# Kernel tuning notes

Measured on AMD Instinct MI355X. Metric: run time of the kernel, lower is better.

The kernel has to match this reference:

```python
import jax, jax.numpy as jnp
import numpy as np
from jax import lax

PS = 4  # patchsize

def conv2d(x, w, b, pad, dil=1):
    y = lax.conv_general_dilated(x, w, (1, 1), [(pad, pad), (pad, pad)],
                                 rhs_dilation=(dil, dil),
                                 dimension_numbers=('NCHW', 'OIHW', 'NCHW'))
    return y + b[None, :, None, None]

def instance_norm(x, eps=1e-5):
    mu = x.mean(axis=(2, 3), keepdims=True)
    var = x.var(axis=(2, 3), keepdims=True)
    return (x - mu) / jnp.sqrt(var + eps)

def lrelu(x):
    return jnp.where(x >= 0, x, 0.2 * x)

def setup_inputs() -> dict:
    key = jax.random.key(0)
    ks = jax.random.split(key, 20)
    B, C, H, W = 16, 256, 64, 64
    nh, nw = H // PS, W // PS
    N = nh * nw
    s = 0.05
    return {
        'x': jax.random.normal(ks[0], (B, C, H, W), jnp.float32),
        'mask': jax.random.uniform(ks[1], (B, 1, H, W), jnp.float32),
        'dis': jax.random.normal(ks[2], (N, N), jnp.float32),
        'lap_a': jnp.ones((1,), jnp.float32),
        'Wq': jax.random.normal(ks[3], (C, C, 1, 1), jnp.float32) * s,
        'bq': jax.random.normal(ks[4], (C,), jnp.float32) * s,
        'Wk': jax.random.normal(ks[5], (C, C, 1, 1), jnp.float32) * s,
        'bk': jax.random.normal(ks[6], (C,), jnp.float32) * s,
        'Wv': jax.random.normal(ks[7], (C, C, 1, 1), jnp.float32) * s,
        'bv': jax.random.normal(ks[8], (C,), jnp.float32) * s,
        'noise_q': jax.random.normal(ks[9], (B, C, nh, PS, nw, PS), jnp.float32),
        'noise_k': jax.random.normal(ks[10], (B, C, nh, PS, nw, PS), jnp.float32),
        'noise_v': jax.random.normal(ks[11], (B, C, nh, PS, nw, PS), jnp.float32),
        'W_out': jax.random.normal(ks[12], (C, C, 3, 3), jnp.float32) * s,
        'b_out': jax.random.normal(ks[13], (C,), jnp.float32) * s,
        'W1': jax.random.normal(ks[14], (C, C, 3, 3), jnp.float32) * s,
        'b1': jax.random.normal(ks[15], (C,), jnp.float32) * s,
        'W2': jax.random.normal(ks[16], (C, C, 3, 3), jnp.float32) * s,
        'b2': jax.random.normal(ks[17], (C,), jnp.float32) * s,
    }

def _patchify(t, noise, B, C, nh, nw):
    # (B,C,H,W) -> (B,C,nh,PS,nw,PS) + noise -> (B, nh*nw, C*PS*PS)
    t = t.reshape(B, C, nh, PS, nw, PS) + noise
    t = t.transpose(0, 2, 4, 1, 3, 5).reshape(B, nh * nw, C * PS * PS)
    return t

def reference(x, mask, dis, lap_a, Wq, bq, Wk, bk, Wv, bv,
              noise_q, noise_k, noise_v, W_out, b_out, W1, b1, W2, b2):
    B, C, H, W = x.shape
    nh, nw = H // PS, W // PS
    N = nh * nw
    head = PS * 4
    Cp = C * PS * PS
    d = Cp // head

    residual = x
    q = _patchify(conv2d(x, Wq, bq, 0), noise_q, B, C, nh, nw)
    k = _patchify(conv2d(x, Wk, bk, 0), noise_k, B, C, nh, nw)
    v = _patchify(conv2d(x, Wv, bv, 0), noise_v, B, C, nh, nw)

    dis_b = jax.nn.softplus(lap_a)[0] * dis  # (N, N)

    qh = q.reshape(B, N, head, d)
    kh = k.reshape(B, N, head, d)
    vh = v.reshape(B, N, head, d)

    # scores: (head, B, N, N); bias added BEFORE scaling, as in the original
    scores = jnp.einsum('bnhd,bmhd->hbnm', qh, kh)
    scores = (scores + dis_b) / jnp.sqrt(jnp.asarray(d, scores.dtype))

    # mask: patch mean < 0.5 masks key positions
    m = mask.reshape(B, 1, nh, PS, nw, PS).transpose(0, 2, 4, 1, 3, 5)
    m = m.reshape(B, N, PS * PS).mean(-1) < 0.5  # (B, N) bool
    m = jnp.broadcast_to(m[:, None, :], (B, N, N))  # (B, N, N)
    scores = jnp.where(m[None], -jnp.inf, scores)

    p = jax.nn.softmax(scores, axis=-1)
    out = jnp.einsum('hbnm,bmhd->bnhd', p, vh).reshape(B, N, Cp)

    # un-patchify: (B,N,Cp) -> (B,nh,nw,C,PS,PS) -> (B,C,H,W)
    out = out.reshape(B, nh, nw, C, PS, PS).transpose(0, 3, 1, 4, 2, 5).reshape(B, C, H, W)
    out = lrelu(conv2d(out, W_out, b_out, 1)) + residual

    # feed-forward: conv(dil=2) -> IN -> lrelu -> conv -> IN -> lrelu, residual
    y = lrelu(instance_norm(conv2d(out, W1, b1, 2, dil=2)))
    y = lrelu(instance_norm(conv2d(y, W2, b2, 1)))
    return out + y
```

## Files before the change

### kernel.cpp

```cpp
#include <hip/hip_runtime.h>
#include <cstdint>
#include <cstddef>

typedef _Float16 f16;
typedef _Float16 f16x8 __attribute__((ext_vector_type(8)));
typedef _Float16 f16x4 __attribute__((ext_vector_type(4)));
typedef float    f32x4 __attribute__((ext_vector_type(4)));

#define MFMA16(a,b,c) __builtin_amdgcn_mfma_f32_16x16x32_f16((a),(b),(c),0,0,0)

__device__ __forceinline__ float lrelu(float v){ return v >= 0.f ? v : 0.2f*v; }


__global__ __launch_bounds__(256) void k_prep1x1(
    const float* __restrict__ wq, const float* __restrict__ wk, const float* __restrict__ wv,
    f16* __restrict__ oq, f16* __restrict__ ok, f16* __restrict__ ov)
{
  int i = blockIdx.x*256 + threadIdx.x;
  int sel = i >> 16, r = i & 65535;
  const float* s = sel==0 ? wq : (sel==1 ? wk : wv);
  f16* d = sel==0 ? oq : (sel==1 ? ok : ov);
  d[r] = (f16)s[r];
}

__global__ __launch_bounds__(256) void k_prep3x3(
    const float* __restrict__ w0, const float* __restrict__ w1, const float* __restrict__ w2,
    f16* __restrict__ o0, f16* __restrict__ o1, f16* __restrict__ o2)
{
  int i = blockIdx.x*256 + threadIdx.x;
  int sel = i / 589824;
  int r = i - sel*589824;
  int t = r >> 16; int rr = r & 65535; int co = rr >> 8; int ci = rr & 255;
  const float* s = sel==0 ? w0 : (sel==1 ? w1 : w2);
  f16* d = sel==0 ? o0 : (sel==1 ? o1 : o2);
  d[r] = (f16)s[(co*256 + ci)*9 + t];
}

__global__ __launch_bounds__(256) void k_pmask(const float* __restrict__ mask, float* __restrict__ pm)
{
  int t = blockIdx.x*256 + threadIdx.x;
  int b = t >> 8, n = t & 255;
  int y0 = (n>>4)<<2, x0 = (n&15)<<2;
  const float* mb = mask + b*4096;
  float s = 0.f;
  #pragma unroll
  for (int i=0;i<4;++i)
    #pragma unroll
    for (int j=0;j<4;++j) s += mb[(y0+i)*64 + x0+j];
  pm[t] = (s*(1.f/16.f) < 0.5f) ? 1.f : 0.f;
}

__global__ __launch_bounds__(256) void k_nchw2nhwc(
    const float* __restrict__ src, const float2* __restrict__ st, f16* __restrict__ dst)
{
  int idx = blockIdx.x;
  int y = idx & 63, b = idx >> 6;
  int tid = threadIdx.x;
  __shared__ f16 T[64*264];

  {
    const float* row = src + (size_t)(b*256+tid)*4096 + y*64;
    float mu = 0.f, ri = 1.f;
    bool doin = (st != nullptr);
    if (doin){ float2 s = st[b*256+tid]; mu = s.x; ri = s.y; }
    #pragma unroll
    for (int j=0;j<16;++j){
      float4 u = *(const float4*)(row + j*4);
      int x = j*4;
      float a0=(u.x-mu)*ri, a1=(u.y-mu)*ri, a2=(u.z-mu)*ri, a3=(u.w-mu)*ri;
      if (doin){ a0=lrelu(a0); a1=lrelu(a1); a2=lrelu(a2); a3=lrelu(a3); }
      T[(x+0)*264+tid]=(f16)a0; T[(x+1)*264+tid]=(f16)a1;
      T[(x+2)*264+tid]=(f16)a2; T[(x+3)*264+tid]=(f16)a3;
    }
  }
  __syncthreads();
  {
    int oct = tid & 31, pxl = tid >> 5;
    #pragma unroll
    for (int p=0;p<8;++p){
      int px = p*8 + pxl;
      *(uint4*)&dst[((size_t)((b*64+y)*64+px)<<8) + oct*8] = *(const uint4*)&T[px*264 + oct*8];
    }
  }
}

__global__ __launch_bounds__(256) void k_qkv(
    const f16* __restrict__ xh,
    const f16* __restrict__ wq, const f16* __restrict__ wk, const f16* __restrict__ wv,
    const float* __restrict__ bq, const float* __restrict__ bk, const float* __restrict__ bv,
    const float* __restrict__ nq, const float* __restrict__ nk, const float* __restrict__ nv,
    f16* __restrict__ Qp, f16* __restrict__ Kp, f16* __restrict__ Vt)
{
  int idx = blockIdx.x;
  int yt  = idx & 15; idx >>= 4;
  int cot = idx & 3;  idx >>= 2;
  int b   = idx & 15; idx >>= 4;
  int sel = idx;
  int tid = threadIdx.x;
  int wave = tid>>6, lane = tid&63, quad = lane>>4, l16 = lane&15;
  int co0 = cot*64, y0 = yt*4;

  const f16*  W    = sel==0 ? wq : (sel==1 ? wk : wv);
  const float* bias= sel==0 ? bq : (sel==1 ? bk : bv);
  const float* nz  = sel==0 ? nq : (sel==1 ? nk : nv);

  __shared__ f16 smem[64*264];
  f16* Al = smem;
  f16* Bl = smem + 2560;

  f32x4 acc[16];
  #pragma unroll
  for (int i=0;i<16;++i){ acc[i][0]=0.f; acc[i][1]=0.f; acc[i][2]=0.f; acc[i][3]=0.f; }

  for (int kc=0;kc<8;++kc){
    int ci0 = kc*32;
    {
      int aco = tid>>2, ap = (tid&3)*8;
      *(uint4*)&Al[aco*40+ap] = *(const uint4*)&W[((co0+aco)<<8) + ci0 + ap];
    }
    #pragma unroll
    for (int p=0;p<4;++p){
      int i = p*256 + tid;
      int px = i>>2, oct = i&3;
      uint4 v = *(const uint4*)&xh[((size_t)((b*64 + y0 + (px>>6))*64 + (px&63))<<8) + ci0 + oct*8];
      *(uint4*)&Bl[px*32 + ((oct ^ (px&3))<<3)] = v;
    }
    __syncthreads();
    f16x8 af = *(const f16x8*)&Al[(wave*16+l16)*40 + quad*8];
    #pragma unroll
    for (int nt=0;nt<16;++nt){
      int bidx = (nt>>2)*64 + (nt&3)*16 + l16;
      f16x8 bf = *(const f16x8*)&Bl[bidx*32 + ((quad ^ (bidx&3))<<3)];
      acc[nt] = MFMA16(af, bf, acc[nt]);
    }
    __syncthreads();
  }

  int cob = co0 + wave*16 + quad*4;
  int h0 = cot*4, pr = yt;
  #pragma unroll
  for (int nt=0;nt<16;++nt){
    int y = y0 + (nt>>2), x = (nt&3)*16 + l16;
    int n_ = (nt&3)*4 + (l16>>2);
    int ddb = (quad<<6) + ((nt>>2)<<2) + (l16&3);
    #pragma unroll
    for (int r=0;r<4;++r){
      int co = cob + r;
      float v = acc[nt][r] + bias[co] + nz[(size_t)(b*256+co)*4096 + y*64 + x];
      int dd = ddb + (r<<4);
      if (sel < 2) smem[(wave*16 + n_)*264 + dd] = (f16)v;
      else         smem[(wave<<12) + (dd<<4) + n_] = (f16)v;
    }
  }
  __syncthreads();
  if (sel < 2){
    f16* dst = sel==0 ? Qp : Kp;
    #pragma unroll
    for (int pass=0; pass<8; ++pass){
      int row = pass*8 + (tid>>5);
      int ch  = tid & 31;
      uint4 v = *(const uint4*)&smem[row*264 + ch*8];
      *(uint4*)&dst[((b*16 + h0 + (row>>4))<<16) + ((pr*16 + (row&15))<<8) + ch*8] = v;
    }
  } else {
    #pragma unroll
    for (int pass=0; pass<8; ++pass){
      int i = pass*256 + tid;
      int rw = i>>1, half = i&1;
      uint4 v = *(const uint4*)&smem[(rw<<4) + (half<<3)];
      *(uint4*)&Vt[((b*16 + h0 + (rw>>8))<<16) + ((rw&255)<<8) + pr*16 + (half<<3)] = v;
    }
  }
}

__global__ __launch_bounds__(256) void k_attn(
    const f16* __restrict__ Qp, const f16* __restrict__ Kp, const f16* __restrict__ Vt,
    const float* __restrict__ dis, const float* __restrict__ lap_a,
    const float* __restrict__ pm, f16* __restrict__ attn)
{
  int idx = blockIdx.x;
  int nt = idx & 3; idx >>= 2;
  int h  = idx & 15; idx >>= 4;
  int b  = idx;
  int tid = threadIdx.x, wave = tid>>6, lane = tid&63, quad = lane>>4, l16 = lane&15;
  int n0 = nt*64;
  int bh = (b*16 + h) << 16;

  __shared__ f16 smem[25344];
  f16* Ql  = smem;
  f16* KVl = smem + 16896;

  {
    int row = tid>>2, part = (tid&3)*64;
    const uint4* s = (const uint4*)&Qp[bh + ((n0+row)<<8) + part];
    uint4* d = (uint4*)&Ql[row*264 + part];
    #pragma unroll
    for (int j=0;j<8;++j) d[j] = s[j];
  }

  float splus = log1pf(expf(lap_a[0]));

  f32x4 sacc[16];
  #pragma unroll
  for (int i=0;i<16;++i){ sacc[i][0]=0.f; sacc[i][1]=0.f; sacc[i][2]=0.f; sacc[i][3]=0.f; }

  #pragma unroll
  for (int mc=0; mc<8; ++mc){
    __syncthreads();
    {
      int row = tid>>3, part = (tid&7)*32;
      const uint4* s = (const uint4*)&Kp[bh + ((mc*32+row)<<8) + part];
      uint4* d = (uint4*)&KVl[row*264 + part];
      #pragma unroll
      for (int j=0;j<4;++j) d[j] = s[j];
    }
    __syncthreads();
    #pragma unroll
    for (int kk=0;kk<8;++kk){
      f16x8 af = *(const f16x8*)&Ql[(wave*16+l16)*264 + kk*32 + quad*8];
      #pragma unroll
      for (int j=0;j<2;++j){
        f16x8 bf = *(const f16x8*)&KVl[(j*16+l16)*264 + kk*32 + quad*8];
        sacc[mc*2+j] = MFMA16(af, bf, sacc[mc*2+j]);
      }
    }
  }

  int nrow_base = wave*16 + quad*4;
  float pmv[16];
  #pragma unroll
  for (int t=0;t<16;++t) pmv[t] = pm[b*256 + t*16 + l16];

  #pragma unroll
  for (int r=0;r<4;++r){
    int n = n0 + nrow_base + r;
    float sv[16];
    float mx = -1e30f;
    #pragma unroll
    for (int t=0;t<16;++t){
      float s = sacc[t][r];
      s = (s + splus * dis[n*256 + t*16 + l16]) * 0.0625f;
      s = (pmv[t] > 0.5f) ? -1e30f : s;
      sv[t] = s;
      mx = fmaxf(mx, s);
    }
    #pragma unroll
    for (int off=1; off<16; off<<=1) mx = fmaxf(mx, __shfl_xor(mx, off, 64));
    float sum = 0.f;
    #pragma unroll
    for (int t=0;t<16;++t){ float e = __expf(sv[t]-mx); sv[t]=e; sum += e; }
    #pragma unroll
    for (int off=1; off<16; off<<=1) sum += __shfl_xor(sum, off, 64);
    float inv = 1.f/sum;
    #pragma unroll
    for (int t=0;t<16;++t) Ql[(nrow_base + r)*264 + t*16 + l16] = (f16)(sv[t]*inv);
  }

  f32x4 oacc[16];
  #pragma unroll
  for (int i=0;i<16;++i){ oacc[i][0]=0.f; oacc[i][1]=0.f; oacc[i][2]=0.f; oacc[i][3]=0.f; }

  for (int dc=0; dc<8; ++dc){
    __syncthreads();
    {
      int row = tid>>3, part = (tid&7)*32;
      const uint4* s = (const uint4*)&Vt[bh + ((dc*32+row)<<8) + part];
      uint4* d = (uint4*)&KVl[row*264 + part];
      #pragma unroll
      for (int j=0;j<4;++j) d[j] = s[j];
    }
    __syncthreads();
    #pragma unroll
    for (int kk=0;kk<8;++kk){
      f16x8 af = *(const f16x8*)&Ql[(wave*16+l16)*264 + kk*32 + quad*8];
      #pragma unroll
      for (int j=0;j<2;++j){
        f16x8 bf = *(const f16x8*)&KVl[(j*16+l16)*264 + kk*32 + quad*8];
        oacc[dc*2+j] = MFMA16(af, bf, oacc[dc*2+j]);
      }
    }
  }

  __syncthreads();
  #pragma unroll
  for (int dc=0; dc<8; ++dc){
    #pragma unroll
    for (int j=0;j<2;++j){
      int dd = dc*32 + j*16 + l16;
      int c_ = dd>>4;
      int pi = (dd>>2)&3, pj = dd&3;
      #pragma unroll
      for (int r=0;r<4;++r){
        int nl = nrow_base + r;
        int y_ = ((nl>>4)<<2) + pi;
        int x  = ((nl&15)<<2) + pj;
        smem[(y_*64 + x)*24 + c_] = (f16)oacc[dc*2+j][r];
      }
    }
  }
  __syncthreads();
  #pragma unroll
  for (int p=0;p<4;++p){
    int pix = p*256 + tid;
    int y_ = pix>>6, x = pix&63;
    uint4 v0 = *(const uint4*)&smem[pix*24];
    uint4 v1 = *(const uint4*)&smem[pix*24 + 8];
    size_t o = ((size_t)((b*64 + nt*16 + y_)*64 + x)<<8) + h*16;
    *(uint4*)&attn[o]     = v0;
    *(uint4*)&attn[o + 8] = v1;
  }
}

template<int DIL, int MODE>
__global__ __launch_bounds__(256) void k_conv3(
    const f16* __restrict__ in, const f16* __restrict__ Wt, const float* __restrict__ bias,
    const float* __restrict__ resid, float* __restrict__ outf, f16* __restrict__ outh)
{
  int idx = blockIdx.x;
  int yt  = idx & 15; idx >>= 4;
  int cot = idx & 3;  idx >>= 2;
  int b   = idx;
  int y0 = yt*4, co0 = cot*64;
  int tid = threadIdx.x;
  int wave = tid>>6, lane = tid&63, quad = lane>>4, l16 = lane&15;

  __shared__ f16 Al[3*64*40];
  __shared__ f16 Bl[4*68*32];

  f32x4 acc[16];
  #pragma unroll
  for (int i=0;i<16;++i){ acc[i][0]=0.f; acc[i][1]=0.f; acc[i][2]=0.f; acc[i][3]=0.f; }

  constexpr int PXR = 64 + 2*DIL;
  constexpr int NU4 = 16*PXR;

  for (int ky=0; ky<3; ++ky){
    int yb = y0 + DIL*(ky-1);
    for (int kc=0; kc<8; ++kc){
      int ci0 = kc*32;
      {
        int aco = tid>>2, ap = (tid&3)*8;
        #pragma unroll
        for (int kx=0;kx<3;++kx)
          *(uint4*)&Al[kx*2560 + aco*40 + ap] =
              *(const uint4*)&Wt[((ky*3+kx)<<16) + ((co0+aco)<<8) + ci0 + ap];
      }
      #pragma unroll
      for (int p=0;p<5;++p){
        int i = p*256 + tid;
        if (i < NU4){
          int px = i>>2, oct = i&3;
          int yr = px / PXR, xp = px - yr*PXR;
          int yy = yb + yr, xx = xp - DIL;
          uint4 v = make_uint4(0u,0u,0u,0u);
          if (yy>=0 && yy<64 && xx>=0 && xx<64)
            v = *(const uint4*)&in[((size_t)((b*64+yy)*64+xx)<<8) + ci0 + oct*8];
          int si = yr*68 + xp;
          *(uint4*)&Bl[si*32 + ((oct ^ (si&3))<<3)] = v;
        }
      }
      __syncthreads();
      #pragma unroll
      for (int kx=0;kx<3;++kx){
        f16x8 af = *(const f16x8*)&Al[kx*2560 + (wave*16+l16)*40 + quad*8];
        #pragma unroll
        for (int nt=0;nt<16;++nt){
          int bidx = (nt>>2)*68 + (nt&3)*16 + l16 + kx*DIL;
          f16x8 bf = *(const f16x8*)&Bl[bidx*32 + ((quad ^ (bidx&3))<<3)];
          acc[nt] = MFMA16(af, bf, acc[nt]);
        }
      }
      __syncthreads();
    }
  }

  int cob = co0 + wave*16 + quad*4;
  float bs[4];
  #pragma unroll
  for (int r=0;r<4;++r) bs[r] = bias[cob+r];
  #pragma unroll
  for (int nt=0;nt<16;++nt){
    int y = y0 + (nt>>2), x = (nt&3)*16 + l16;
    #pragma unroll
    for (int r=0;r<4;++r){
      int co = cob + r;
      float v = acc[nt][r] + bs[r];
      size_t o = (size_t)(b*256+co)*4096 + y*64 + x;
      if (MODE==0){
        v = lrelu(v) + resid[o];
        outf[o] = v;
        outh[((size_t)((b*64+y)*64+x)<<8) + co] = (f16)v;
      } else {
        outf[o] = v;
      }
    }
  }
}

__global__ __launch_bounds__(256) void k_instats(const float* __restrict__ v, float2* __restrict__ st)
{
  int bc = blockIdx.x;
  const float* p = v + (size_t)bc*4096;
  int tid = threadIdx.x;
  float s=0.f, ss=0.f;
  #pragma unroll
  for (int it=0; it<4; ++it){
    float4 u = *(const float4*)(p + it*1024 + tid*4);
    s  += u.x+u.y+u.z+u.w;
    ss += u.x*u.x + u.y*u.y + u.z*u.z + u.w*u.w;
  }
  #pragma unroll
  for (int off=32; off; off>>=1){ s += __shfl_down(s, off, 64); ss += __shfl_down(ss, off, 64); }
  __shared__ float rs[4], rss[4];
  int wave = tid>>6, lane = tid&63;
  if (lane==0){ rs[wave]=s; rss[wave]=ss; }
  __syncthreads();
  if (tid==0){
    float S = rs[0]+rs[1]+rs[2]+rs[3], SS = rss[0]+rss[1]+rss[2]+rss[3];
    float mu = S*(1.f/4096.f);
    float var = SS*(1.f/4096.f) - mu*mu;
    st[bc] = make_float2(mu, rsqrtf(var + 1e-5f));
  }
}

__global__ __launch_bounds__(256) void k_final(float* __restrict__ out, const float* __restrict__ c2,
                                               const float2* __restrict__ st)
{
  int i4 = blockIdx.x*256 + threadIdx.x;
  float2 s = st[i4>>10];
  float4 u = *(const float4*)(c2 + (size_t)i4*4);
  float4 o = *(const float4*)(out + (size_t)i4*4);
  o.x += lrelu((u.x - s.x)*s.y);
  o.y += lrelu((u.y - s.x)*s.y);
  o.z += lrelu((u.z - s.x)*s.y);
  o.w += lrelu((u.w - s.x)*s.y);
  *(float4*)(out + (size_t)i4*4) = o;
}

extern "C" void kernel_launch(void* const* d_in, const int* in_sizes, int n_in,
                              void* d_out, int out_size, void* d_ws, size_t ws_size,
                              hipStream_t stream)
{
  const float* x    = (const float*)d_in[0];
  const float* mask = (const float*)d_in[1];
  const float* dis  = (const float*)d_in[2];
  const float* lapa = (const float*)d_in[3];
  const float* Wq   = (const float*)d_in[4];
  const float* bq   = (const float*)d_in[5];
  const float* Wk   = (const float*)d_in[6];
  const float* bk   = (const float*)d_in[7];
  const float* Wv   = (const float*)d_in[8];
  const float* bv   = (const float*)d_in[9];
  const float* nq   = (const float*)d_in[10];
  const float* nk   = (const float*)d_in[11];
  const float* nv   = (const float*)d_in[12];
  const float* Wo   = (const float*)d_in[13];
  const float* bo   = (const float*)d_in[14];
  const float* W1   = (const float*)d_in[15];
  const float* b1   = (const float*)d_in[16];
  const float* W2   = (const float*)d_in[17];
  const float* b2   = (const float*)d_in[18];

  char* w = (char*)d_ws;
  f16*   xh    = (f16*)(w + 0);
  f16*   Qp    = (f16*)(w + 33554432);
  f16*   Kp    = (f16*)(w + 67108864);
  f16*   Vt    = (f16*)(w + 100663296);
  f16*   attnb = (f16*)(w + 134217728);
  f16*   outbf = (f16*)(w + 0);
  float* c1    = (float*)(w + 33554432);
  f16*   y1    = (f16*)(w + 100663296);
  float* c2    = (float*)(w + 33554432);
  f16*   wqh   = (f16*)(w + 167772160);
  f16*   wkh   = wqh + 65536;
  f16*   wvh   = wkh + 65536;
  f16*   wt0   = (f16*)(w + 168165376);
  f16*   wt1   = wt0 + 589824;
  f16*   wt2   = wt1 + 589824;
  float* pmk   = (float*)(w + 171704320);
  float2* st1  = (float2*)(w + 171720704);
  float2* st2  = (float2*)(w + 171753472);
  float* out   = (float*)d_out;

  k_prep1x1<<<768, 256, 0, stream>>>(Wq, Wk, Wv, wqh, wkh, wvh);
  k_prep3x3<<<6912, 256, 0, stream>>>(Wo, W1, W2, wt0, wt1, wt2);
  k_pmask<<<16, 256, 0, stream>>>(mask, pmk);
  k_nchw2nhwc<<<1024, 256, 0, stream>>>(x, nullptr, xh);
  k_qkv<<<3072, 256, 0, stream>>>(xh, wqh, wkh, wvh, bq, bk, bv, nq, nk, nv, Qp, Kp, Vt);
  k_attn<<<1024, 256, 0, stream>>>(Qp, Kp, Vt, dis, lapa, pmk, attnb);
  k_conv3<1,0><<<1024, 256, 0, stream>>>(attnb, wt0, bo, x, out, outbf);
  k_conv3<2,1><<<1024, 256, 0, stream>>>(outbf, wt1, b1, nullptr, c1, nullptr);
  k_instats<<<4096, 256, 0, stream>>>(c1, st1);
  k_nchw2nhwc<<<1024, 256, 0, stream>>>(c1, st1, y1);
  k_conv3<1,1><<<1024, 256, 0, stream>>>(y1, wt2, b2, nullptr, c2, nullptr);
  k_instats<<<4096, 256, 0, stream>>>(c2, st2);
  k_final<<<16384, 256, 0, stream>>>(out, c2, st2);
}
```

Baseline: 1.070 ms.

## Double-buffer QKV projection tiles with async global-to-LDS loads

Replaces the synchronous register-staged loads of weight and activation tiles in the QKV 1x1 projection kernel with direct global_load_lds async copies into a double-buffered LDS layout. The next K-chunk is prefetched while MFMAs run on the current one, using explicit vmcnt waits and barriers. The swizzle pattern changes to match the 16-byte-per-lane direct-to-LDS write layout. This adds LDS usage and relies on hand-tuned waitcnt values being correct.

```diff
diff --git a/kernel.cpp b/kernel.cpp
--- a/kernel.cpp
+++ b/kernel.cpp
@@ -10,6 +10,13 @@
 #define MFMA16(a,b,c) __builtin_amdgcn_mfma_f32_16x16x32_f16((a),(b),(c),0,0,0)
 
 __device__ __forceinline__ float lrelu(float v){ return v >= 0.f ? v : 0.2f*v; }
+
+__device__ __forceinline__ void async_copy16(const f16* g, f16* l){
+  __builtin_amdgcn_global_load_lds(
+      (const __attribute__((address_space(1))) void*)(uintptr_t)(const void*)g,
+      (__attribute__((address_space(3))) void*)(uint32_t)(uintptr_t)(void*)l,
+      16, 0, 0);
+}
 
 
 __global__ __launch_bounds__(256) void k_prep1x1(
@@ -104,36 +111,48 @@
   const float* bias= sel==0 ? bq : (sel==1 ? bk : bv);
   const float* nz  = sel==0 ? nq : (sel==1 ? nk : nv);
 
-  __shared__ f16 smem[64*264];
-  f16* Al = smem;
-  f16* Bl = smem + 2560;
+  __shared__ f16 smem[20480];
 
   f32x4 acc[16];
   #pragma unroll
   for (int i=0;i<16;++i){ acc[i][0]=0.f; acc[i][1]=0.f; acc[i][2]=0.f; acc[i][3]=0.f; }
 
-  for (int kc=0;kc<8;++kc){
-    int ci0 = kc*32;
-    {
-      int aco = tid>>2, ap = (tid&3)*8;
-      *(uint4*)&Al[aco*40+ap] = *(const uint4*)&W[((co0+aco)<<8) + ci0 + ap];
-    }
-    #pragma unroll
-    for (int p=0;p<4;++p){
-      int i = p*256 + tid;
-      int px = i>>2, oct = i&3;
-      uint4 v = *(const uint4*)&xh[((size_t)((b*64 + y0 + (px>>6))*64 + (px&63))<<8) + ci0 + oct*8];
-      *(uint4*)&Bl[px*32 + ((oct ^ (px&3))<<3)] = v;
-    }
-    __syncthreads();
-    f16x8 af = *(const f16x8*)&Al[(wave*16+l16)*40 + quad*8];
+  int g8 = (((lane&3) ^ ((lane>>3)&3)) << 3);
+  const f16* Wrow = W + ((co0 + wave*16 + (lane>>2))<<8) + g8;
+  const f16* Xrow = xh + (((size_t)((b*64 + y0)*64))<<8) + g8;
+
+  auto stage = [&](int buf, int kc){
+    int ci0 = kc<<5;
+    f16* Ab = smem + buf*2048;
+    f16* Bb = smem + 4096 + buf*8192;
+    async_copy16(Wrow + ci0, Ab + wave*512);
+    #pragma unroll
+    for (int j=0;j<4;++j){
+      int px = j*64 + wave*16 + (lane>>2);
+      async_copy16(Xrow + ((size_t)px<<8) + ci0, Bb + (j*64 + wave*16)*32);
+    }
+  };
+
+  stage(0, 0);
+  #pragma unroll
+  for (int kc=0; kc<8; ++kc){
+    int cur = kc & 1;
+    if (kc < 7){
+      stage(cur^1, kc+1);
+      asm volatile("s_waitcnt vmcnt(5)\n\ts_barrier" ::: "memory");
+    } else {
+      asm volatile("s_waitcnt vmcnt(0)\n\ts_barrier" ::: "memory");
+    }
+    const f16* Al = smem + cur*2048;
+    const f16* Bl = smem + 4096 + cur*8192;
+    f16x8 af = *(const f16x8*)&Al[(wave*16+l16)*32 + ((quad ^ ((l16>>1)&3))<<3)];
     #pragma unroll
     for (int nt=0;nt<16;++nt){
       int bidx = (nt>>2)*64 + (nt&3)*16 + l16;
-      f16x8 bf = *(const f16x8*)&Bl[bidx*32 + ((quad ^ (bidx&3))<<3)];
+      f16x8 bf = *(const f16x8*)&Bl[bidx*32 + ((quad ^ ((bidx>>1)&3))<<3)];
       acc[nt] = MFMA16(af, bf, acc[nt]);
     }
-    __syncthreads();
+    asm volatile("s_waitcnt lgkmcnt(0)\n\ts_barrier" ::: "memory");
   }
 
   int cob = co0 + wave*16 + quad*4;
```

Measured after the change: 1.068 ms. Within noise of the previous version (-0.2%).
